# Kernel optimization log

Measured on AMD Instinct MI355X. Metric: run time of the kernel, lower is better.

## Reference

```python
import jax, jax.numpy as jnp
import numpy as np

N = 1024
ODE_UNFOLDS = 6
EPS = 1e-8
RICCATI_ITERS = 6  # fixed-point DARE iteration standing in for the (undefined) lqr() helper
MASK_DENSITY = 0.4


def lqr(A, B, Q, R):
    # Discrete-time Riccati iteration: P <- A'PA - A'PB (R+B'PB)^{-1} B'PA + Q
    P = Q
    for _ in range(RICCATI_ITERS):
        BtP = B.T @ P                         # [N,N]
        K = jnp.linalg.solve(R + BtP @ B, BtP @ A)
        P = A.T @ P @ (A - B @ K) + Q
    BtP = B.T @ P
    K = jnp.linalg.solve(R + BtP @ B, BtP @ A)
    return K, P


def setup_inputs() -> dict:
    key = jax.random.key(0)
    ks = jax.random.split(key, 24)
    u = lambda k, shape, lo, hi: jax.random.uniform(k, shape, jnp.float32, lo, hi)
    # sprandsym-style SPD laplacian param, rescaled to [0.001, 1]
    rng = np.random.default_rng(0)
    X = (rng.standard_normal((N, N)) * (rng.random((N, N)) < 0.1)).astype(np.float32)
    A = X @ X.T + 0.01 * np.eye(N, dtype=np.float32)
    A = (A - A.min()) / (A.max() - A.min())
    lap = (A * (1.0 - 0.001) + 0.001).astype(np.float32)

    mask = (jax.random.uniform(ks[2], (N, N)) < MASK_DENSITY).astype(jnp.float32)
    smask = (jax.random.uniform(ks[3], (N, N)) < MASK_DENSITY).astype(jnp.float32)
    return dict(
        inputs=jax.random.normal(ks[0], (N,), jnp.float32),
        adj=jax.random.uniform(ks[1], (N, N), jnp.float32) / N,  # scaled for numerical stability of the Riccati loop
        laplacian=jnp.asarray(lap),
        control=u(ks[6], (N,), 0.001, 4.0),
        gleak=u(ks[7], (N,), 0.001, 1.0),
        vleak=u(ks[8], (N,), -0.2, 0.2),
        cm=u(ks[9], (N,), 0.4, 0.6),
        sigma=u(ks[10], (N, N), 3.0, 8.0),
        mu=u(ks[11], (N, N), 0.3, 0.8),
        w=u(ks[12], (N, N), 0.001, 1.0),
        erev=jnp.sign(jax.random.normal(ks[4], (N, N))) * mask,
        sensory_sigma=u(ks[13], (N, N), 3.0, 8.0),
        sensory_mu=u(ks[14], (N, N), 0.3, 0.8),
        sensory_w=u(ks[15], (N, N), 0.001, 1.0),
        sensory_erev=jnp.sign(jax.random.normal(ks[5], (N, N))) * smask,
        sparsity_mask=mask,
        sensory_sparsity_mask=smask,
        input_w=jnp.ones((N,), jnp.float32),
        input_b=jnp.zeros((N,), jnp.float32),
        output_w=jnp.ones((N,), jnp.float32),
        output_b=jnp.zeros((N,), jnp.float32),
        attn_w=jax.random.normal(ks[16], (N,), jnp.float32) / jnp.sqrt(N),
        attn_b=jax.random.normal(ks[17], (1,), jnp.float32),
        gc_w=jax.random.normal(ks[18], (1, 1), jnp.float32),
        gc_b=jax.random.normal(ks[19], (1,), jnp.float32),
    )


def reference(inputs, adj, laplacian, control, gleak, vleak, cm, sigma, mu, w, erev,
              sensory_sigma, sensory_mu, sensory_w, sensory_erev,
              sparsity_mask, sensory_sparsity_mask,
              input_w, input_b, output_w, output_b, attn_w, attn_b, gc_w, gc_b):
    x = inputs * input_w + input_b                      # _map_inputs (affine)
    n = x.shape[0]

    # ControlAttention with R = Q = eye(N): fc(I) rows = attn_w + attn_b
    att = attn_w + attn_b[0]                            # [N]
    s = x * att
    att_e = jnp.exp(s - jnp.max(s))                     # stable exp weighting
    Qm = jnp.diag(att_e)
    Rm = jnp.diag(att_e)                                # Q_att == R_att since Q == R == I

    K, _ = lqr(adj, laplacian, Qm, Rm)                  # K: [N,N]
    ctrl = (control - jnp.mean(K * x, axis=1)) @ laplacian  # [N]

    # sensory synapse activation (constant over the unfold loop)
    sens_act = sensory_w * jax.nn.sigmoid(sensory_sigma * (x[:, None] - sensory_mu)) * sensory_sparsity_mask
    w_num_s = jnp.sum(sens_act * sensory_erev, axis=1)  # [N]
    w_den_s = jnp.sum(sens_act, axis=1)                 # [N]

    gcn = lambda h: jax.nn.relu(adj @ (h * gc_w[0, 0]) + gc_b[0])
    d = x[:, None]
    for _ in range(4):
        d = gcn(d)
    d = d[:, 0]

    cm_t = d + cm * ODE_UNFOLDS + ctrl                  # elapsed_time = 1.0 -> cm / (1/unfolds)

    v = jnp.zeros((n,), x.dtype)                        # states default: zeros
    for _ in range(ODE_UNFOLDS):
        w_act = w * jax.nn.sigmoid(sigma * (v[:, None] - mu)) * sparsity_mask
        w_num = jnp.sum(w_act * erev, axis=1) + w_num_s
        w_den = jnp.sum(w_act, axis=1) + w_den_s
        v = (cm_t * v + gleak * vleak + w_num) / (cm_t + gleak + w_den + EPS)

    out = v * output_w + output_b                       # motor_size == state_size path
    return out, v, laplacian, ctrl + control
```

## Files before the change

### kernel.cpp

```cpp
#include <hip/hip_runtime.h>

#define MSZ (1024*1024)
#define LD 1024
#define CFS_NB 128


__global__ __launch_bounds__(1024) void prep_k(const float* __restrict__ inp, const float* __restrict__ iw,
    const float* __restrict__ ib, const float* __restrict__ aw, const float* __restrict__ ab,
    float* __restrict__ xv, float* __restrict__ atte) {
  __shared__ float red[1024];
  int t = threadIdx.x;
  float x = inp[t] * iw[t] + ib[t];
  float s = x * (aw[t] + ab[0]);
  xv[t] = x;
  red[t] = s;
  __syncthreads();
  for (int o = 512; o > 0; o >>= 1) { if (t < o) red[t] = fmaxf(red[t], red[t + o]); __syncthreads(); }
  atte[t] = expf(s - red[0]);
}

__global__ void setdiag_k(float* __restrict__ P, const float* __restrict__ atte) {
  int idx = blockIdx.x * 256 + threadIdx.x;
  int r = idx >> 10, c = idx & 1023;
  P[idx] = (r == c) ? atte[r] : 0.0f;
}

__global__ __launch_bounds__(256) void sens_k(const float* __restrict__ sw, const float* __restrict__ ssig,
    const float* __restrict__ smu, const float* __restrict__ serev, const float* __restrict__ smask,
    const float* __restrict__ xv, float* __restrict__ wns, float* __restrict__ wds) {
  __shared__ float rn[256], rd[256];
  int i = blockIdx.x, t = threadIdx.x;
  float xi = xv[i];
  float n = 0.f, d = 0.f;
  for (int j = t; j < 1024; j += 256) {
    int idx = i * 1024 + j;
    float z = ssig[idx] * (xi - smu[idx]);
    float sg = 1.0f / (1.0f + expf(-z));
    float act = sw[idx] * sg * smask[idx];
    n += act * serev[idx];
    d += act;
  }
  rn[t] = n; rd[t] = d;
  __syncthreads();
  for (int o = 128; o > 0; o >>= 1) { if (t < o) { rn[t] += rn[t + o]; rd[t] += rd[t + o]; } __syncthreads(); }
  if (t == 0) { wns[i] = rn[0]; wds[i] = rd[0]; }
}

__global__ __launch_bounds__(256) void gcn_k(const float* __restrict__ adj, const float* __restrict__ hin,
    float* __restrict__ hout, const float* __restrict__ gcw, const float* __restrict__ gcb) {
  __shared__ float red[256];
  int i = blockIdx.x, t = threadIdx.x;
  float s = 0.f;
  for (int j = t; j < 1024; j += 256) s += adj[(size_t)i * 1024 + j] * hin[j];
  red[t] = s; __syncthreads();
  for (int o = 128; o > 0; o >>= 1) { if (t < o) red[t] += red[t + o]; __syncthreads(); }
  if (t == 0) hout[i] = fmaxf(gcw[0] * red[0] + gcb[0], 0.0f);
}

__global__ __launch_bounds__(256) void matvec_n_k(const float* __restrict__ M, const float* __restrict__ v,
    float* __restrict__ out) {
  __shared__ float red[256];
  int i = blockIdx.x, t = threadIdx.x;
  float s = 0.f;
  for (int j = t; j < 1024; j += 256) s += M[(size_t)i * 1024 + j] * v[j];
  red[t] = s; __syncthreads();
  for (int o = 128; o > 0; o >>= 1) { if (t < o) red[t] += red[t + o]; __syncthreads(); }
  if (t == 0) out[i] = red[0];
}

__global__ __launch_bounds__(256) void matvec_t_k(const float* __restrict__ M, const float* __restrict__ v,
    float* __restrict__ out) {
  int j = blockIdx.x * 256 + threadIdx.x;
  float s = 0.f;
  #pragma unroll 8
  for (int i = 0; i < 1024; i++) s += M[(size_t)i * 1024 + j] * v[i];
  out[j] = s;
}

__global__ void gctrl_k(const float* __restrict__ control, const float* __restrict__ u, float* __restrict__ g) {
  int t = blockIdx.x * 256 + threadIdx.x;
  g[t] = control[t] - u[t] * (1.0f / 1024.0f);
}

__global__ void copylap_k(const float4* __restrict__ src, float4* __restrict__ dst) {
  int i = blockIdx.x * 256 + threadIdx.x;
  dst[i] = src[i];
}


struct GDesc { const float* A; const float* B; float* C; const float* diag; int tri; int mode; };
struct GArgs { GDesc d[3]; };

template<int TA>
__global__ __launch_bounds__(256) void gemm64x128_k(GArgs ga) {
  GDesc de = ga.d[blockIdx.z];
  int row0 = blockIdx.y * 64, col0 = blockIdx.x * 128;
  if (de.tri && row0 + 64 <= col0) return;
  __shared__ float As[32][64];
  __shared__ float Bs[32][128];
  const float* __restrict__ A = de.A;
  const float* __restrict__ B = de.B;
  int t = threadIdx.x;
  int tx = t & 15, ty = t >> 4;
  float acc[4][8] = {};
  for (int k0 = 0; k0 < 1024; k0 += 32) {
    if (TA == 1) {
      #pragma unroll
      for (int h = 0; h < 2; h++) {
        int s = h * 256 + t;
        int bk = s >> 4, am = (s & 15) * 4;
        float4 v = *(const float4*)(A + (size_t)(k0 + bk) * LD + row0 + am);
        *(float4*)(&As[bk][am]) = v;
      }
    } else {
      #pragma unroll
      for (int h = 0; h < 2; h++) {
        int s = h * 256 + t;
        int am = s >> 3, k4 = (s & 7) * 4;
        float4 v = *(const float4*)(A + (size_t)(row0 + am) * LD + k0 + k4);
        As[k4 + 0][am] = v.x; As[k4 + 1][am] = v.y; As[k4 + 2][am] = v.z; As[k4 + 3][am] = v.w;
      }
    }
    #pragma unroll
    for (int h = 0; h < 4; h++) {
      int s = h * 256 + t;
      int bk = s >> 5, bn = (s & 31) * 4;
      float4 v = *(const float4*)(B + (size_t)(k0 + bk) * LD + col0 + bn);
      *(float4*)(&Bs[bk][bn]) = v;
    }
    __syncthreads();
    #pragma unroll
    for (int k = 0; k < 32; k++) {
      float4 a4 = *(float4*)(&As[k][tx * 4]);
      float4 b0 = *(float4*)(&Bs[k][ty * 8]);
      float4 b1 = *(float4*)(&Bs[k][ty * 8 + 4]);
      float a[4] = {a4.x, a4.y, a4.z, a4.w};
      float b[8] = {b0.x, b0.y, b0.z, b0.w, b1.x, b1.y, b1.z, b1.w};
      #pragma unroll
      for (int i = 0; i < 4; i++)
        #pragma unroll
        for (int j = 0; j < 8; j++)
          acc[i][j] += a[i] * b[j];
    }
    __syncthreads();
  }
  #pragma unroll
  for (int i = 0; i < 4; i++) {
    int gm = row0 + tx * 4 + i;
    if (de.diag) {
      int dc = gm - col0 - ty * 8;
      if (dc >= 0 && dc < 8) acc[i][dc] += de.diag[gm];
    }
    float* cp = de.C + (size_t)gm * LD + col0 + ty * 8;
    if (de.mode == 0) {
      float4 o0 = {acc[i][0], acc[i][1], acc[i][2], acc[i][3]};
      float4 o1 = {acc[i][4], acc[i][5], acc[i][6], acc[i][7]};
      *(float4*)cp = o0; *(float4*)(cp + 4) = o1;
    } else {
      float4 c0 = *(float4*)cp, c1 = *(float4*)(cp + 4);
      c0.x -= acc[i][0]; c0.y -= acc[i][1]; c0.z -= acc[i][2]; c0.w -= acc[i][3];
      c1.x -= acc[i][4]; c1.y -= acc[i][5]; c1.z -= acc[i][6]; c1.w -= acc[i][7];
      *(float4*)cp = c0; *(float4*)(cp + 4) = c1;
    }
  }
}


__device__ __forceinline__ void gsync(int* bar) {
  __syncthreads();
  if (threadIdx.x == 0) {
    __threadfence();
    int gen = __hip_atomic_load(bar + 1, __ATOMIC_RELAXED, __HIP_MEMORY_SCOPE_AGENT);
    int n = __hip_atomic_fetch_add(bar, 1, __ATOMIC_RELAXED, __HIP_MEMORY_SCOPE_AGENT);
    if (n + 1 == (int)gridDim.x) {
      __hip_atomic_store(bar, 0, __ATOMIC_RELAXED, __HIP_MEMORY_SCOPE_AGENT);
      __hip_atomic_store(bar + 1, gen + 1, __ATOMIC_RELAXED, __HIP_MEMORY_SCOPE_AGENT);
    } else {
      while (__hip_atomic_load(bar + 1, __ATOMIC_RELAXED, __HIP_MEMORY_SCOPE_AGENT) == gen) {
        __builtin_amdgcn_s_sleep(16);
      }
    }
    __threadfence();
  }
  __syncthreads();
}

__device__ __forceinline__ void potf2_lds(float (*T)[132], int l, float r[64]) {
  #pragma unroll
  for (int k = 0; k < 64; k++) r[k] = T[l][k];
  #pragma unroll
  for (int j = 0; j < 64; j++) {
    float dj = __shfl(r[j], j, 64);
    float Ljj = sqrtf(fmaxf(dj, 1e-12f));
    float inv = 1.0f / Ljj;
    if (l == j) r[j] = Ljj;
    else if (l > j) r[j] *= inv;
    #pragma unroll
    for (int k = j + 1; k < 64; k++) {
      float Lkj = __shfl(r[j], k, 64);
      r[k] -= r[j] * Lkj;
    }
  }
}

__global__ __launch_bounds__(256) void cfs_k(float* __restrict__ Mm, float* __restrict__ Lb,
                                             float* __restrict__ S, int* __restrict__ bar) {
  __shared__ float shA[64][68];
  __shared__ float shB[64][132];
  int t = threadIdx.x;
  int bid = blockIdx.x;
  int nb = gridDim.x;

  if (bid == 0) {
    #pragma unroll
    for (int h = 0; h < 4; h++) {
      int q = h * 256 + t, r = q >> 4, c4 = (q & 15) * 4;
      *(float4*)(&shB[r][c4]) = *(const float4*)(Mm + (size_t)r * LD + c4);
    }
    __syncthreads();
    if (t < 64) {
      float r[64];
      potf2_lds(shB, t, r);
      #pragma unroll
      for (int k = 0; k < 64; k++) if (k <= t) Lb[(size_t)t * LD + k] = r[k];
    }
  }
  gsync(bar);

  for (int s = 0; s < 16; s++) {
    int e = s * 64, e2 = e + 64, nt = 15 - s, rb = nt * 64;
    int nPanel = (rb + 255) / 256;
    int nRhs = S ? 4 : 0;
    int njA = nPanel + nRhs;
    if (bid < njA) {
      #pragma unroll
      for (int h = 0; h < 4; h++) {
        int q = h * 256 + t, r = q >> 4, c4 = (q & 15) * 4;
        *(float4*)(&shA[r][c4]) = *(const float4*)(Lb + (size_t)(e + r) * LD + e + c4);
      }
      __syncthreads();
      if (bid < nPanel) {
        int row = e2 + bid * 256 + t;
        if (row < 1024) {
          float y[64];
          #pragma unroll
          for (int k = 0; k < 64; k++) y[k] = Mm[(size_t)row * LD + e + k];
          #pragma unroll
          for (int kk = 0; kk < 64; kk++) {
            float v = y[kk];
            #pragma unroll
            for (int m = 0; m < kk; m++) v -= shA[kk][m] * y[m];
            y[kk] = v / shA[kk][kk];
          }
          #pragma unroll
          for (int k = 0; k < 64; k++) Lb[(size_t)row * LD + e + k] = y[k];
        }
      } else {
        int col = (bid - nPanel) * 256 + t;
        float y[64];
        #pragma unroll
        for (int k = 0; k < 64; k++) y[k] = S[(size_t)(e + k) * LD + col];
        #pragma unroll
        for (int kk = 0; kk < 64; kk++) {
          float v = y[kk];
          #pragma unroll
          for (int m = 0; m < kk; m++) v -= shA[kk][m] * y[m];
          y[kk] = v / shA[kk][kk];
        }
        #pragma unroll
        for (int k = 0; k < 64; k++) S[(size_t)(e + k) * LD + col] = y[k];
      }
    }
    gsync(bar);
    if (nt > 0) {
      if (bid == 0) {
        #pragma unroll
        for (int h = 0; h < 4; h++) {
          int q = h * 256 + t, r = q >> 4, c4 = (q & 15) * 4;
          *(float4*)(&shA[r][c4]) = *(const float4*)(Lb + (size_t)(e2 + r) * LD + e + c4);
        }
        __syncthreads();
        for (int idx = t; idx < 4096; idx += 256) {
          int r = idx >> 6, c = idx & 63;
          float a = Mm[(size_t)(e2 + r) * LD + e2 + c];
          #pragma unroll
          for (int k = 0; k < 64; k++) a -= shA[r][k] * shA[c][k];
          shB[r][c] = a;
        }
        __syncthreads();
        if (t < 64) {
          float r[64];
          potf2_lds(shB, t, r);
          #pragma unroll
          for (int k = 0; k < 64; k++) if (k <= t) Lb[(size_t)(e2 + t) * LD + e2 + k] = r[k];
        }
      } else {
        int nSyrk = nt * (nt + 1) / 2 - 1;
        int nSupd = S ? nt * 8 : 0;
        int njB = nSyrk + nSupd;
        for (int job = bid - 1; job < njB; job += nb - 1) {
          if (job < nSyrk) {
            int q = job + 1;
            int i0 = (int)((sqrtf(8.0f * q + 1.0f) - 1.0f) * 0.5f);
            while ((i0 + 1) * (i0 + 2) / 2 <= q) i0++;
            while (i0 * (i0 + 1) / 2 > q) i0--;
            int j0 = q - i0 * (i0 + 1) / 2;
            int ra = e + 64 * (i0 + 1), rc = e + 64 * (j0 + 1);
            #pragma unroll
            for (int h = 0; h < 4; h++) {
              int qq = h * 256 + t, r = qq >> 4, c4 = (qq & 15) * 4;
              *(float4*)(&shA[r][c4]) = *(const float4*)(Lb + (size_t)(ra + r) * LD + e + c4);
              *(float4*)(&shB[r][c4]) = *(const float4*)(Lb + (size_t)(rc + r) * LD + e + c4);
            }
            __syncthreads();
            int tx = t & 15, ty = t >> 4;
            float acc[4][4] = {};
            #pragma unroll 8
            for (int k = 0; k < 64; k++) {
              float a[4], b[4];
              #pragma unroll
              for (int i = 0; i < 4; i++) a[i] = shA[tx * 4 + i][k];
              #pragma unroll
              for (int j = 0; j < 4; j++) b[j] = shB[ty * 4 + j][k];
              #pragma unroll
              for (int i = 0; i < 4; i++)
                #pragma unroll
                for (int j = 0; j < 4; j++)
                  acc[i][j] += a[i] * b[j];
            }
            #pragma unroll
            for (int i = 0; i < 4; i++) {
              float* cp = Mm + (size_t)(ra + tx * 4 + i) * LD + rc + ty * 4;
              float4 c = *(float4*)cp;
              c.x -= acc[i][0]; c.y -= acc[i][1]; c.z -= acc[i][2]; c.w -= acc[i][3];
              *(float4*)cp = c;
            }
            __syncthreads();
          } else {
            int q = job - nSyrk;
            int i0 = (q >> 3) + 1, cb = q & 7;
            int ra = e + 64 * i0, c0 = cb * 128;
            #pragma unroll
            for (int h = 0; h < 4; h++) {
              int qq = h * 256 + t, r = qq >> 4, c4 = (qq & 15) * 4;
              *(float4*)(&shA[r][c4]) = *(const float4*)(Lb + (size_t)(ra + r) * LD + e + c4);
            }
            #pragma unroll
            for (int h = 0; h < 8; h++) {
              int qq = h * 256 + t, r = qq >> 5, c4 = (qq & 31) * 4;
              *(float4*)(&shB[r][c4]) = *(const float4*)(S + (size_t)(e + r) * LD + c0 + c4);
            }
            __syncthreads();
            int tx = t & 15, ty = t >> 4;
            float acc[4][8] = {};
            #pragma unroll 8
            for (int k = 0; k < 64; k++) {
              float a[4];
              #pragma unroll
              for (int i = 0; i < 4; i++) a[i] = shA[tx * 4 + i][k];
              float4 b0 = *(float4*)(&shB[k][ty * 8]);
              float4 b1 = *(float4*)(&shB[k][ty * 8 + 4]);
              float b[8] = {b0.x, b0.y, b0.z, b0.w, b1.x, b1.y, b1.z, b1.w};
              #pragma unroll
              for (int i = 0; i < 4; i++)
                #pragma unroll
                for (int j = 0; j < 8; j++)
                  acc[i][j] += a[i] * b[j];
            }
            #pragma unroll
            for (int i = 0; i < 4; i++) {
              float* cp = S + (size_t)(ra + tx * 4 + i) * LD + c0 + ty * 8;
              float4 v0 = *(float4*)cp, v1 = *(float4*)(cp + 4);
              v0.x -= acc[i][0]; v0.y -= acc[i][1]; v0.z -= acc[i][2]; v0.w -= acc[i][3];
              v1.x -= acc[i][4]; v1.y -= acc[i][5]; v1.z -= acc[i][6]; v1.w -= acc[i][7];
              *(float4*)cp = v0; *(float4*)(cp + 4) = v1;
            }
            __syncthreads();
          }
        }
      }
    }
    gsync(bar);
  }
}

__global__ __launch_bounds__(256) void mirror_k(float* __restrict__ P, const float* __restrict__ atte) {
  __shared__ float tile[64][65];
  int b = blockIdx.x, t = threadIdx.x;
  int ti, tj;
  if (b < 16) { ti = b; tj = b; }
  else {
    int p = b - 16;
    ti = (int)((1.0f + sqrtf(1.0f + 8.0f * p)) * 0.5f);
    while (ti * (ti - 1) / 2 > p) ti--;
    while ((ti + 1) * ti / 2 <= p) ti++;
    tj = p - ti * (ti - 1) / 2;
  }
  #pragma unroll
  for (int h = 0; h < 4; h++) {
    int s = h * 256 + t;
    int r = s >> 4, c4 = (s & 15) * 4;
    *(float4*)(&tile[r][c4]) = *(const float4*)(P + (size_t)(ti * 64 + r) * LD + tj * 64 + c4);
  }
  __syncthreads();
  if (ti == tj) {
    #pragma unroll
    for (int h = 0; h < 4; h++) {
      int s = h * 256 + t;
      int r = s >> 4, c4 = (s & 15) * 4;
      #pragma unroll
      for (int j = 0; j < 4; j++) {
        int c = c4 + j;
        if (c > r) P[(size_t)(ti * 64 + r) * LD + tj * 64 + c] = tile[c][r];
        else if (c == r) P[(size_t)(ti * 64 + r) * LD + tj * 64 + c] = tile[r][r] + atte[ti * 64 + r];
      }
    }
  } else {
    #pragma unroll
    for (int h = 0; h < 4; h++) {
      int s = h * 256 + t;
      int r = s >> 4, c4 = (s & 15) * 4;
      float4 o = {tile[c4 + 0][r], tile[c4 + 1][r], tile[c4 + 2][r], tile[c4 + 3][r]};
      *(float4*)(P + (size_t)(tj * 64 + r) * LD + ti * 64 + c4) = o;
    }
  }
}


__global__ __launch_bounds__(1024) void trsv_fwd_k(const float* __restrict__ Lg, const float* __restrict__ bin,
    float* __restrict__ wout) {
  __shared__ float zs[1024];
  __shared__ float wsb[64];
  int t = threadIdx.x;
  zs[t] = bin[t];
  __syncthreads();
  for (int s = 0; s < 16; s++) {
    int e = s * 64;
    if (t < 64) {
      float rr[64];
      #pragma unroll
      for (int k = 0; k < 64; k++) rr[k] = Lg[(size_t)(e + t) * LD + e + k];
      float acc = zs[e + t];
      #pragma unroll
      for (int k = 0; k < 64; k++) {
        float cand = acc / rr[k];
        float wk = __shfl(cand, k, 64);
        if (t == k) wsb[k] = wk;
        if (t > k) acc -= rr[k] * wk;
      }
    }
    __syncthreads();
    if (t < 64) zs[e + t] = wsb[t];
    __syncthreads();
    if (t >= e + 64) {
      float a = zs[t];
      #pragma unroll
      for (int k = 0; k < 64; k++) a -= Lg[(size_t)t * LD + e + k] * wsb[k];
      zs[t] = a;
    }
    __syncthreads();
  }
  wout[t] = zs[t];
}

__global__ __launch_bounds__(1024) void trsv_bwd_k(const float* __restrict__ Lg, const float* __restrict__ bin,
    float* __restrict__ wout) {
  __shared__ float zs[1024];
  __shared__ float wsb[64];
  int t = threadIdx.x;
  zs[t] = bin[t];
  __syncthreads();
  for (int s = 15; s >= 0; s--) {
    int e = s * 64;
    if (t < 64) {
      float rr[64];
      #pragma unroll
      for (int k = 0; k < 64; k++) rr[k] = Lg[(size_t)(e + k) * LD + e + t];
      float acc = zs[e + t];
      #pragma unroll
      for (int k = 63; k >= 0; k--) {
        float cand = acc / rr[k];
        float wk = __shfl(cand, k, 64);
        if (t == k) wsb[k] = wk;
        if (t < k) acc -= rr[k] * wk;
      }
    }
    __syncthreads();
    if (t < 64) zs[e + t] = wsb[t];
    __syncthreads();
    if (t < e) {
      float a = zs[t];
      #pragma unroll
      for (int k = 0; k < 64; k++) a -= Lg[(size_t)(e + k) * LD + t] * wsb[k];
      zs[t] = a;
    }
    __syncthreads();
  }
  wout[t] = zs[t];
}

__global__ __launch_bounds__(256) void ode_k(const float* __restrict__ w, const float* __restrict__ sig,
    const float* __restrict__ mu, const float* __restrict__ erev, const float* __restrict__ mask,
    const float* __restrict__ gleak, const float* __restrict__ vleak, const float* __restrict__ cm,
    const float* __restrict__ dvec, const float* __restrict__ ctrlv, const float* __restrict__ wns,
    const float* __restrict__ wds, const float* __restrict__ ow, const float* __restrict__ ob,
    const float* __restrict__ control, float* __restrict__ dout) {
  __shared__ float wm[1024], we[1024], sgs[1024], mus[1024];
  __shared__ float red[512];
  __shared__ float vsh;
  int i = blockIdx.x, t = threadIdx.x;
  for (int j = t; j < 1024; j += 256) {
    int idx = i * 1024 + j;
    float wmv = w[idx] * mask[idx];
    wm[j] = wmv;
    we[j] = wmv * erev[idx];
    sgs[j] = sig[idx];
    mus[j] = mu[idx];
  }
  float cmt = dvec[i] + cm[i] * 6.0f + ctrlv[i];
  float gl = gleak[i], vl = vleak[i];
  float numS = wns[i], denS = wds[i];
  float v = 0.0f;
  __syncthreads();
  for (int u = 0; u < 6; u++) {
    float n = 0.f, d = 0.f;
    for (int j = t; j < 1024; j += 256) {
      float sgm = 1.0f / (1.0f + expf(-sgs[j] * (v - mus[j])));
      n += we[j] * sgm;
      d += wm[j] * sgm;
    }
    red[t] = n; red[256 + t] = d;
    __syncthreads();
    for (int o = 128; o > 0; o >>= 1) {
      if (t < o) { red[t] += red[t + o]; red[256 + t] += red[256 + t + o]; }
      __syncthreads();
    }
    if (t == 0) {
      float num = red[0] + numS, den = red[256] + denS;
      vsh = (cmt * v + gl * vl + num) / (cmt + gl + den + 1e-8f);
    }
    __syncthreads();
    v = vsh;
    __syncthreads();
  }
  if (t == 0) {
    dout[i] = v * ow[i] + ob[i];
    dout[1024 + i] = v;
    dout[2048 + 1048576 + i] = ctrlv[i] + control[i];
  }
}


extern "C" void kernel_launch(void* const* d_in, const int* in_sizes, int n_in,
                              void* d_out, int out_size, void* d_ws, size_t ws_size,
                              hipStream_t stream) {
  const float* inputs  = (const float*)d_in[0];
  const float* adj     = (const float*)d_in[1];
  const float* lap     = (const float*)d_in[2];
  const float* control = (const float*)d_in[3];
  const float* gleak   = (const float*)d_in[4];
  const float* vleak   = (const float*)d_in[5];
  const float* cm      = (const float*)d_in[6];
  const float* sigma   = (const float*)d_in[7];
  const float* mu      = (const float*)d_in[8];
  const float* w       = (const float*)d_in[9];
  const float* erev    = (const float*)d_in[10];
  const float* ssig    = (const float*)d_in[11];
  const float* smu     = (const float*)d_in[12];
  const float* sw      = (const float*)d_in[13];
  const float* serev   = (const float*)d_in[14];
  const float* mask    = (const float*)d_in[15];
  const float* smask   = (const float*)d_in[16];
  const float* iw      = (const float*)d_in[17];
  const float* ib      = (const float*)d_in[18];
  const float* ow      = (const float*)d_in[19];
  const float* ob      = (const float*)d_in[20];
  const float* aw      = (const float*)d_in[21];
  const float* ab      = (const float*)d_in[22];
  const float* gcw     = (const float*)d_in[23];
  const float* gcb     = (const float*)d_in[24];
  float* out = (float*)d_out;
  float* ws = (float*)d_ws;

  float* P0 = ws;
  float* P1 = ws + (size_t)MSZ;
  float* PA = ws + 2 * (size_t)MSZ;
  float* PB = ws + 3 * (size_t)MSZ;
  float* Mm = ws + 4 * (size_t)MSZ;
  float* S  = ws + 5 * (size_t)MSZ;
  float* vb = ws + 6 * (size_t)MSZ;
  float* xv = vb;            float* atte = vb + 1024;
  float* wns = vb + 2048;    float* wds  = vb + 3072;
  float* dA  = vb + 4096;    float* dB   = vb + 5120;
  float* yv  = vb + 6144;    float* tv   = vb + 7168;
  float* zv  = vb + 8192;    float* wv   = vb + 9216;
  float* uv  = vb + 10240;   float* gv   = vb + 11264;
  float* ctrlv = vb + 12288;
  int*   bar = (int*)(vb + 16384);

  hipMemsetAsync(bar, 0, 2 * sizeof(int), stream);

  prep_k<<<1, 1024, 0, stream>>>(inputs, iw, ib, aw, ab, xv, atte);
  setdiag_k<<<4096, 256, 0, stream>>>(P0, atte);
  sens_k<<<1024, 256, 0, stream>>>(sw, ssig, smu, serev, smask, xv, wns, wds);
  gcn_k<<<1024, 256, 0, stream>>>(adj, xv, dA, gcw, gcb);
  gcn_k<<<1024, 256, 0, stream>>>(adj, dA, dB, gcw, gcb);
  gcn_k<<<1024, 256, 0, stream>>>(adj, dB, dA, gcw, gcb);
  gcn_k<<<1024, 256, 0, stream>>>(adj, dA, dB, gcw, gcb);

  float* P = P0; float* Pn = P1;
  for (int it = 0; it < 6; it++) {
    GArgs g1 = {{ {P, adj, PA, nullptr, 0, 0}, {P, lap, PB, nullptr, 0, 0}, {nullptr,nullptr,nullptr,nullptr,0,0} }};
    gemm64x128_k<0><<<dim3(8, 16, 2), 256, 0, stream>>>(g1);
    GArgs g2 = {{ {PB, adj, S, nullptr, 0, 0}, {PB, lap, Mm, atte, 1, 0}, {adj, PA, Pn, nullptr, 1, 0} }};
    gemm64x128_k<1><<<dim3(8, 16, 3), 256, 0, stream>>>(g2);
    cfs_k<<<CFS_NB, 256, 0, stream>>>(Mm, PA, S, bar);
    GArgs g3 = {{ {S, S, Pn, nullptr, 1, 1}, {nullptr,nullptr,nullptr,nullptr,0,0}, {nullptr,nullptr,nullptr,nullptr,0,0} }};
    gemm64x128_k<1><<<dim3(8, 16, 1), 256, 0, stream>>>(g3);
    mirror_k<<<136, 256, 0, stream>>>(Pn, atte);
    float* tmp = P; P = Pn; Pn = tmp;
  }

  GArgs g4 = {{ {P, lap, PB, nullptr, 0, 0}, {nullptr,nullptr,nullptr,nullptr,0,0}, {nullptr,nullptr,nullptr,nullptr,0,0} }};
  gemm64x128_k<0><<<dim3(8, 16, 1), 256, 0, stream>>>(g4);
  GArgs g5 = {{ {PB, lap, Mm, atte, 1, 0}, {nullptr,nullptr,nullptr,nullptr,0,0}, {nullptr,nullptr,nullptr,nullptr,0,0} }};
  gemm64x128_k<1><<<dim3(8, 16, 1), 256, 0, stream>>>(g5);
  cfs_k<<<CFS_NB, 256, 0, stream>>>(Mm, PA, nullptr, bar);
  matvec_n_k<<<1024, 256, 0, stream>>>(adj, xv, yv);
  matvec_n_k<<<1024, 256, 0, stream>>>(P, yv, tv);
  matvec_t_k<<<4, 256, 0, stream>>>(lap, tv, zv);
  trsv_fwd_k<<<1, 1024, 0, stream>>>(PA, zv, wv);
  trsv_bwd_k<<<1, 1024, 0, stream>>>(PA, wv, uv);
  gctrl_k<<<4, 256, 0, stream>>>(control, uv, gv);
  matvec_t_k<<<4, 256, 0, stream>>>(lap, gv, ctrlv);

  ode_k<<<1024, 256, 0, stream>>>(w, sigma, mu, erev, mask, gleak, vleak, cm, dB, ctrlv,
                                  wns, wds, ow, ob, control, out);
  copylap_k<<<1024, 256, 0, stream>>>((const float4*)lap, (float4*)(out + 2048));
}
```

Measured before the change: 16.54 ms.

## Replace atomic-counter grid barrier with flag-based master barrier; register-tile diagonal SYRK

Swaps the single-counter atomic grid barrier in the blocked Cholesky kernel for a per-block flag scheme. Each block writes its own padded flag, block 0 polls all of them in parallel threads, then releases everyone through one broadcast flag with a monotonic generation. This is meant to cut contention and latency on the 48 barriers per Cholesky. It also restructures block 0's diagonal-tile SYRK update into a 4x4 register-tiled outer product on LDS, staging the Mm tile into shared memory first. The barrier area is now larger and is zeroed with a memset before every cfs launch, which adds an extra memset per call.

```diff
diff --git a/kernel.cpp b/kernel.cpp
--- a/kernel.cpp
+++ b/kernel.cpp
@@ -166,23 +166,31 @@
 }
 
 
-__device__ __forceinline__ void gsync(int* bar) {
+__device__ __forceinline__ void gsync(int* __restrict__ bar, int gen) {
+  int t = threadIdx.x;
+  int nb = gridDim.x;
   __syncthreads();
-  if (threadIdx.x == 0) {
-    __threadfence();
-    int gen = __hip_atomic_load(bar + 1, __ATOMIC_RELAXED, __HIP_MEMORY_SCOPE_AGENT);
-    int n = __hip_atomic_fetch_add(bar, 1, __ATOMIC_RELAXED, __HIP_MEMORY_SCOPE_AGENT);
-    if (n + 1 == (int)gridDim.x) {
-      __hip_atomic_store(bar, 0, __ATOMIC_RELAXED, __HIP_MEMORY_SCOPE_AGENT);
-      __hip_atomic_store(bar + 1, gen + 1, __ATOMIC_RELAXED, __HIP_MEMORY_SCOPE_AGENT);
-    } else {
-      while (__hip_atomic_load(bar + 1, __ATOMIC_RELAXED, __HIP_MEMORY_SCOPE_AGENT) == gen) {
-        __builtin_amdgcn_s_sleep(16);
-      }
-    }
-    __threadfence();
-  }
-  __syncthreads();
+  if (blockIdx.x == 0) {
+    if (t >= 1 && t < nb) {
+      while (__hip_atomic_load(bar + t * 32, __ATOMIC_RELAXED, __HIP_MEMORY_SCOPE_AGENT) < gen)
+        __builtin_amdgcn_s_sleep(2);
+    }
+    __syncthreads();
+    if (t == 0) {
+      __threadfence();
+      __hip_atomic_store(bar + nb * 32, gen, __ATOMIC_RELAXED, __HIP_MEMORY_SCOPE_AGENT);
+    }
+    __syncthreads();
+  } else {
+    if (t == 0) {
+      __threadfence();
+      __hip_atomic_store(bar + blockIdx.x * 32, gen, __ATOMIC_RELAXED, __HIP_MEMORY_SCOPE_AGENT);
+      while (__hip_atomic_load(bar + nb * 32, __ATOMIC_RELAXED, __HIP_MEMORY_SCOPE_AGENT) < gen)
+        __builtin_amdgcn_s_sleep(8);
+      __threadfence();
+    }
+    __syncthreads();
+  }
 }
 
 __device__ __forceinline__ void potf2_lds(float (*T)[132], int l, float r[64]) {
@@ -210,6 +218,7 @@
   int t = threadIdx.x;
   int bid = blockIdx.x;
   int nb = gridDim.x;
+  int gen = 0;
 
   if (bid == 0) {
     #pragma unroll
@@ -225,7 +234,7 @@
       for (int k = 0; k < 64; k++) if (k <= t) Lb[(size_t)t * LD + k] = r[k];
     }
   }
-  gsync(bar);
+  gsync(bar, ++gen);
 
   for (int s = 0; s < 16; s++) {
     int e = s * 64, e2 = e + 64, nt = 15 - s, rb = nt * 64;
@@ -271,21 +280,37 @@
         for (int k = 0; k < 64; k++) S[(size_t)(e + k) * LD + col] = y[k];
       }
     }
-    gsync(bar);
+    gsync(bar, ++gen);
     if (nt > 0) {
       if (bid == 0) {
         #pragma unroll
         for (int h = 0; h < 4; h++) {
           int q = h * 256 + t, r = q >> 4, c4 = (q & 15) * 4;
           *(float4*)(&shA[r][c4]) = *(const float4*)(Lb + (size_t)(e2 + r) * LD + e + c4);
+          *(float4*)(&shB[r][c4]) = *(const float4*)(Mm + (size_t)(e2 + r) * LD + e2 + c4);
         }
         __syncthreads();
-        for (int idx = t; idx < 4096; idx += 256) {
-          int r = idx >> 6, c = idx & 63;
-          float a = Mm[(size_t)(e2 + r) * LD + e2 + c];
+        {
+          int tx = t & 15, ty = t >> 4;
+          float acc[4][4] = {};
+          #pragma unroll 8
+          for (int k = 0; k < 64; k++) {
+            float a[4], b[4];
+            #pragma unroll
+            for (int i = 0; i < 4; i++) a[i] = shA[tx * 4 + i][k];
+            #pragma unroll
+            for (int j = 0; j < 4; j++) b[j] = shA[ty * 4 + j][k];
+            #pragma unroll
+            for (int i = 0; i < 4; i++)
+              #pragma unroll
+              for (int j = 0; j < 4; j++)
+                acc[i][j] += a[i] * b[j];
+          }
           #pragma unroll
-          for (int k = 0; k < 64; k++) a -= shA[r][k] * shA[c][k];
-          shB[r][c] = a;
+          for (int i = 0; i < 4; i++)
+            #pragma unroll
+            for (int j = 0; j < 4; j++)
+              shB[tx * 4 + i][ty * 4 + j] -= acc[i][j];
         }
         __syncthreads();
         if (t < 64) {
@@ -380,7 +405,7 @@
         }
       }
     }
-    gsync(bar);
+    gsync(bar, ++gen);
   }
 }
 
@@ -598,7 +623,7 @@
   float* ctrlv = vb + 12288;
   int*   bar = (int*)(vb + 16384);
 
-  hipMemsetAsync(bar, 0, 2 * sizeof(int), stream);
+  const size_t barBytes = (size_t)(CFS_NB + 1) * 32 * sizeof(int);
 
   prep_k<<<1, 1024, 0, stream>>>(inputs, iw, ib, aw, ab, xv, atte);
   setdiag_k<<<4096, 256, 0, stream>>>(P0, atte);
@@ -614,6 +639,7 @@
     gemm64x128_k<0><<<dim3(8, 16, 2), 256, 0, stream>>>(g1);
     GArgs g2 = {{ {PB, adj, S, nullptr, 0, 0}, {PB, lap, Mm, atte, 1, 0}, {adj, PA, Pn, nullptr, 1, 0} }};
     gemm64x128_k<1><<<dim3(8, 16, 3), 256, 0, stream>>>(g2);
+    hipMemsetAsync(bar, 0, barBytes, stream);
     cfs_k<<<CFS_NB, 256, 0, stream>>>(Mm, PA, S, bar);
     GArgs g3 = {{ {S, S, Pn, nullptr, 1, 1}, {nullptr,nullptr,nullptr,nullptr,0,0}, {nullptr,nullptr,nullptr,nullptr,0,0} }};
     gemm64x128_k<1><<<dim3(8, 16, 1), 256, 0, stream>>>(g3);
@@ -625,6 +651,7 @@
   gemm64x128_k<0><<<dim3(8, 16, 1), 256, 0, stream>>>(g4);
   GArgs g5 = {{ {PB, lap, Mm, atte, 1, 0}, {nullptr,nullptr,nullptr,nullptr,0,0}, {nullptr,nullptr,nullptr,nullptr,0,0} }};
   gemm64x128_k<1><<<dim3(8, 16, 1), 256, 0, stream>>>(g5);
+  hipMemsetAsync(bar, 0, barBytes, stream);
   cfs_k<<<CFS_NB, 256, 0, stream>>>(Mm, PA, nullptr, bar);
   matvec_n_k<<<1024, 256, 0, stream>>>(adj, xv, yv);
   matvec_n_k<<<1024, 256, 0, stream>>>(P, yv, tv);
```

After: 15.75 ms. 1.05x faster.
